# Performance work log

Measured on AMD Instinct MI355X. Metric: run time of the kernel, lower is better.

Reference implementation:

```python
import jax, jax.numpy as jnp
from jax import lax
import numpy as np

T, B, I, H = 365, 2048, 9, 50


def setup_inputs() -> dict:
    key = jax.random.key(0)
    ks = jax.random.split(key, 12)
    s = 0.1
    return {
        "x": jax.random.normal(ks[0], (T, B, I), dtype=jnp.float32),
        "w_ih0": jax.random.normal(ks[1], (4 * H, I), dtype=jnp.float32) * s,
        "w_hh0": jax.random.normal(ks[2], (4 * H, H), dtype=jnp.float32) * s,
        "b_ih0": jax.random.normal(ks[3], (4 * H,), dtype=jnp.float32) * s,
        "b_hh0": jax.random.normal(ks[4], (4 * H,), dtype=jnp.float32) * s,
        "w_ih1": jax.random.normal(ks[5], (4 * H, H), dtype=jnp.float32) * s,
        "w_hh1": jax.random.normal(ks[6], (4 * H, H), dtype=jnp.float32) * s,
        "b_ih1": jax.random.normal(ks[7], (4 * H,), dtype=jnp.float32) * s,
        "b_hh1": jax.random.normal(ks[8], (4 * H,), dtype=jnp.float32) * s,
        "fc_w": jax.random.normal(ks[9], (1, H), dtype=jnp.float32) * s,
        "fc_b": jax.random.normal(ks[10], (1,), dtype=jnp.float32) * s,
    }


def _lstm_layer(x, w_ih, w_hh, b_ih, b_hh):
    # x: [T, B, in]; PyTorch gate order: i, f, g, o
    Bq = x.shape[1]
    Hh = w_hh.shape[1]
    # precompute input projections for all timesteps (one big GEMM)
    x_proj = jnp.einsum('tbi,gi->tbg', x, w_ih) + b_ih + b_hh  # [T, B, 4H]

    def step(carry, xp):
        h, c = carry
        gates = xp + h @ w_hh.T  # [B, 4H]
        i, f, g, o = jnp.split(gates, 4, axis=-1)
        i = jax.nn.sigmoid(i)
        f = jax.nn.sigmoid(f)
        g = jnp.tanh(g)
        o = jax.nn.sigmoid(o)
        c = f * c + i * g
        h = o * jnp.tanh(c)
        return (h, c), h

    h0 = jnp.zeros((Bq, Hh), dtype=x.dtype)
    _, hs = lax.scan(step, (h0, h0), x_proj)
    return hs  # [T, B, H]


def reference(x, w_ih0, w_hh0, b_ih0, b_hh0, w_ih1, w_hh1, b_ih1, b_hh1, fc_w, fc_b):
    h1 = _lstm_layer(x, w_ih0, w_hh0, b_ih0, b_hh0)
    h2 = _lstm_layer(h1, w_ih1, w_hh1, b_ih1, b_hh1)
    out = jnp.einsum('tbh,oh->tbo', h2, fc_w) + fc_b  # [T, B, 1]
    return out
```

## Files before the change

### kernel.cpp

```cpp
#include <hip/hip_runtime.h>

#define T_STEPS 365
#define BATCH   2048
#define INP     9
#define HID     50
#define MB      16
#define NBLK    (BATCH/MB)
#define NT      512
#define NTILES  13

typedef __attribute__((ext_vector_type(8))) short short8;
typedef __attribute__((ext_vector_type(4))) float float4v;

__device__ __forceinline__ unsigned short f2bf(float v) {
    unsigned u = __builtin_bit_cast(unsigned, v);
    unsigned r = (u + 0x7FFFu + ((u >> 16) & 1u)) >> 16;
    return (unsigned short)r;
}
__device__ __forceinline__ float sig_(float x) {
    return __builtin_amdgcn_rcpf(1.f + __expf(-x));
}
__device__ __forceinline__ float tanh_(float x) {
    return 1.f - 2.f * __builtin_amdgcn_rcpf(__expf(2.f * x) + 1.f);
}

__device__ __forceinline__ int hx_off(int m, int k) {
    return (m * 128 + k) ^ ((m & 7) << 3);
}

__global__ __launch_bounds__(NT, 2)
void lstm_pipe(const float* __restrict__ x,
               const float* __restrict__ w_ih0, const float* __restrict__ w_hh0,
               const float* __restrict__ b_ih0, const float* __restrict__ b_hh0,
               const float* __restrict__ w_ih1, const float* __restrict__ w_hh1,
               const float* __restrict__ b_ih1, const float* __restrict__ b_hh1,
               const float* __restrict__ fc_w, const float* __restrict__ fc_b,
               float* __restrict__ out)
{
    __shared__ __align__(16) unsigned short HX[2][MB * 128];
    __shared__ float FCP[2][4][MB];

    const int t    = threadIdx.x;
    const int w    = t >> 6;
    const int lid  = t & 63;
    const int mcol = lid & 15;
    const int kgrp = lid >> 4;
    const int kb8  = kgrp * 8;
    const int b0   = blockIdx.x * MB;
    const bool isL1 = (w < 4);
    const int v    = isL1 ? w : (w - 4);
    const float fcb = fc_b[0];

    short8 wA[4][4];
    float  bs[4][4], fcw[4], cst[4];
    const float* bih = isL1 ? b_ih1 : b_ih0;
    const float* bhh = isL1 ? b_hh1 : b_hh0;

    #pragma unroll
    for (int tt = 0; tt < 4; ++tt) {
        const int T  = v + 4 * tt;
        const bool tv = (T < NTILES);
        const int r  = T * 16 + mcol;
        const bool rv = tv && (r < 4 * HID);
        const int u_r = r >> 2, g_r = r & 3;
        const int orig = g_r * HID + u_r;
        if (isL1) {
            #pragma unroll
            for (int kt = 0; kt < 4; ++kt) {
                short8 f;
                #pragma unroll
                for (int j = 0; j < 8; ++j) {
                    int k = kt * 32 + kb8 + j;
                    float val = 0.f;
                    if (rv) {
                        if (k < HID)                      val = w_ih1[orig * HID + k];
                        else if (k >= 64 && k < 64 + HID) val = w_hh1[orig * HID + (k - 64)];
                    }
                    f[j] = (short)f2bf(val);
                }
                wA[tt][kt] = f;
            }
        } else {
            #pragma unroll
            for (int kt = 0; kt < 2; ++kt) {
                short8 f;
                #pragma unroll
                for (int j = 0; j < 8; ++j) {
                    int k = kt * 32 + kb8 + j;
                    float val = 0.f;
                    if (rv) {
                        if (k < HID)            val = w_hh0[orig * HID + k];
                        else if (k < HID + INP) val = w_ih0[orig * INP + (k - HID)];
                    }
                    f[j] = (short)f2bf(val);
                }
                wA[tt][kt] = f;
            }
            wA[tt][2] = short8{}; wA[tt][3] = short8{};
        }
        const int u_lane = T * 4 + kgrp;
        #pragma unroll
        for (int rr = 0; rr < 4; ++rr) {
            int row = T * 16 + kgrp * 4 + rr;
            bool bvv = tv && (row < 4 * HID);
            int uu = row >> 2;
            bs[tt][rr] = bvv ? (bih[rr * HID + uu] + bhh[rr * HID + uu]) : 0.f;
        }
        fcw[tt] = (isL1 && tv && u_lane < HID) ? fc_w[u_lane] : 0.f;
        cst[tt] = 0.f;
    }

    int xi = -1;
    if (w == 4) xi = lid;
    else if (w == 5) xi = 64 + lid;
    else if (w == 6 && lid < 16) xi = 128 + lid;
    const bool xact = (xi >= 0 && xi < MB * INP);
    const int xm = xact ? xi / INP : 0, xj = xact ? xi % INP : 0;

    for (int i = t; i < 2 * MB * 128; i += NT) (&HX[0][0])[i] = 0;
    if (t < 2 * 4 * MB) (&FCP[0][0][0])[t] = 0.f;
    __syncthreads();
    float xreg = 0.f;
    if (xact) {
        HX[1][hx_off(xm, HID + xj)] = f2bf(x[(size_t)(b0 + xm) * INP + xj]);
        xreg = x[((size_t)BATCH + b0 + xm) * INP + xj];
    }
    __syncthreads();

    for (int ph = 0; ph < T_STEPS + 2; ++ph) {
        const int cur = (ph + 1) & 1, nxt = ph & 1;

        short8 f0 = *(const short8*)&HX[cur][hx_off(mcol, kb8)];
        short8 f1 = *(const short8*)&HX[cur][hx_off(mcol, 32 + kb8)];

        if (isL1) {
            if (ph >= 1 && ph <= T_STEPS) {
                short8 f2 = *(const short8*)&HX[cur][hx_off(mcol, 64 + kb8)];
                short8 f3 = *(const short8*)&HX[cur][hx_off(mcol, 96 + kb8)];
                float h1v[4];
                float fcp = 0.f;
                #pragma unroll
                for (int tt = 0; tt < 4; ++tt) {
                    const int T = v + 4 * tt;
                    if (T < NTILES) {
                        float4v acc = {bs[tt][0], bs[tt][1], bs[tt][2], bs[tt][3]};
                        acc = __builtin_amdgcn_mfma_f32_16x16x32_bf16(wA[tt][0], f0, acc, 0, 0, 0);
                        acc = __builtin_amdgcn_mfma_f32_16x16x32_bf16(wA[tt][1], f1, acc, 0, 0, 0);
                        acc = __builtin_amdgcn_mfma_f32_16x16x32_bf16(wA[tt][2], f2, acc, 0, 0, 0);
                        acc = __builtin_amdgcn_mfma_f32_16x16x32_bf16(wA[tt][3], f3, acc, 0, 0, 0);
                        float gi = sig_(acc[0]), gf = sig_(acc[1]);
                        float gg = tanh_(acc[2]), go = sig_(acc[3]);
                        cst[tt] = gf * cst[tt] + gi * gg;
                        h1v[tt] = go * tanh_(cst[tt]);
                        fcp += fcw[tt] * h1v[tt];
                    }
                }
                #pragma unroll
                for (int tt = 0; tt < 4; ++tt) {
                    const int T = v + 4 * tt, u = T * 4 + kgrp;
                    if (T < NTILES && u < HID)
                        HX[nxt][hx_off(mcol, 64 + u)] = f2bf(h1v[tt]);
                }
                fcp += __shfl_xor(fcp, 16);
                fcp += __shfl_xor(fcp, 32);
                if (lid < MB) FCP[ph & 1][v][lid] = fcp;
            }
        } else {
            if (ph < T_STEPS) {
                float h0v[4];
                #pragma unroll
                for (int tt = 0; tt < 4; ++tt) {
                    const int T = v + 4 * tt;
                    if (T < NTILES) {
                        float4v acc = {bs[tt][0], bs[tt][1], bs[tt][2], bs[tt][3]};
                        acc = __builtin_amdgcn_mfma_f32_16x16x32_bf16(wA[tt][0], f0, acc, 0, 0, 0);
                        acc = __builtin_amdgcn_mfma_f32_16x16x32_bf16(wA[tt][1], f1, acc, 0, 0, 0);
                        float gi = sig_(acc[0]), gf = sig_(acc[1]);
                        float gg = tanh_(acc[2]), go = sig_(acc[3]);
                        cst[tt] = gf * cst[tt] + gi * gg;
                        h0v[tt] = go * tanh_(cst[tt]);
                    }
                }
                #pragma unroll
                for (int tt = 0; tt < 4; ++tt) {
                    const int T = v + 4 * tt, u = T * 4 + kgrp;
                    if (T < NTILES && u < HID)
                        HX[nxt][hx_off(mcol, u)] = f2bf(h0v[tt]);
                }
            }
            if (xact) {
                if (ph + 1 < T_STEPS) HX[nxt][hx_off(xm, HID + xj)] = f2bf(xreg);
                if (ph + 2 < T_STEPS) xreg = x[((size_t)(ph + 2) * BATCH + b0 + xm) * INP + xj];
            }
            if (w == 7 && lid < MB && ph >= 2) {
                const int rp = (ph - 1) & 1;
                float s = fcb + FCP[rp][0][lid] + FCP[rp][1][lid]
                              + FCP[rp][2][lid] + FCP[rp][3][lid];
                out[(size_t)(ph - 2) * BATCH + b0 + lid] = s;
            }
        }
        __syncthreads();
    }
}

extern "C" void kernel_launch(void* const* d_in, const int* in_sizes, int n_in,
                              void* d_out, int out_size, void* d_ws, size_t ws_size,
                              hipStream_t stream) {
    const float* x     = (const float*)d_in[0];
    const float* w_ih0 = (const float*)d_in[1];
    const float* w_hh0 = (const float*)d_in[2];
    const float* b_ih0 = (const float*)d_in[3];
    const float* b_hh0 = (const float*)d_in[4];
    const float* w_ih1 = (const float*)d_in[5];
    const float* w_hh1 = (const float*)d_in[6];
    const float* b_ih1 = (const float*)d_in[7];
    const float* b_hh1 = (const float*)d_in[8];
    const float* fc_w  = (const float*)d_in[9];
    const float* fc_b  = (const float*)d_in[10];
    float* out = (float*)d_out;

    lstm_pipe<<<dim3(NBLK), dim3(NT), 0, stream>>>(
        x, w_ih0, w_hh0, b_ih0, b_hh0,
        w_ih1, w_hh1, b_ih1, b_hh1, fc_w, fc_b, out);
}
```

Baseline: 369.8 us.

## Double waves per block to shorten per-step serial tile chain

Blocks grow from 8 to 16 waves. Each layer now gets 8 waves, so each wave handles at most 2 gate tiles instead of 4, which shortens the serial MFMA and activation chain inside each timestep. The layer-1 MFMA chain is also split into two independent accumulators that are summed afterwards, to reduce dependency latency. In exchange the block is larger and the per-step barrier has more participants. The layer-0 waves also keep redundant zero weight registers, and the launch bound becomes (1024, 4), which tightens the per-thread register budget.

```diff
diff --git a/kernel.cpp b/kernel.cpp
--- a/kernel.cpp
+++ b/kernel.cpp
@@ -6,8 +6,9 @@
 #define HID     50
 #define MB      16
 #define NBLK    (BATCH/MB)
-#define NT      512
+#define NT      1024
 #define NTILES  13
+#define TPW     2
 
 typedef __attribute__((ext_vector_type(8))) short short8;
 typedef __attribute__((ext_vector_type(4))) float float4v;
@@ -28,17 +29,17 @@
     return (m * 128 + k) ^ ((m & 7) << 3);
 }
 
-__global__ __launch_bounds__(NT, 2)
-void lstm_pipe(const float* __restrict__ x,
-               const float* __restrict__ w_ih0, const float* __restrict__ w_hh0,
-               const float* __restrict__ b_ih0, const float* __restrict__ b_hh0,
-               const float* __restrict__ w_ih1, const float* __restrict__ w_hh1,
-               const float* __restrict__ b_ih1, const float* __restrict__ b_hh1,
-               const float* __restrict__ fc_w, const float* __restrict__ fc_b,
-               float* __restrict__ out)
+__global__ __launch_bounds__(NT, 4)
+void lstm_pipe16(const float* __restrict__ x,
+                 const float* __restrict__ w_ih0, const float* __restrict__ w_hh0,
+                 const float* __restrict__ b_ih0, const float* __restrict__ b_hh0,
+                 const float* __restrict__ w_ih1, const float* __restrict__ w_hh1,
+                 const float* __restrict__ b_ih1, const float* __restrict__ b_hh1,
+                 const float* __restrict__ fc_w, const float* __restrict__ fc_b,
+                 float* __restrict__ out)
 {
     __shared__ __align__(16) unsigned short HX[2][MB * 128];
-    __shared__ float FCP[2][4][MB];
+    __shared__ float FCP[2][8][MB];
 
     const int t    = threadIdx.x;
     const int w    = t >> 6;
@@ -47,56 +48,42 @@
     const int kgrp = lid >> 4;
     const int kb8  = kgrp * 8;
     const int b0   = blockIdx.x * MB;
-    const bool isL1 = (w < 4);
-    const int v    = isL1 ? w : (w - 4);
+    const bool isL1 = (w < 8);
+    const int v    = w & 7;
     const float fcb = fc_b[0];
 
-    short8 wA[4][4];
-    float  bs[4][4], fcw[4], cst[4];
+    short8 wA[TPW][4];
+    float  bs[TPW][4], fcw[TPW], cst[TPW];
     const float* bih = isL1 ? b_ih1 : b_ih0;
     const float* bhh = isL1 ? b_hh1 : b_hh0;
 
     #pragma unroll
-    for (int tt = 0; tt < 4; ++tt) {
-        const int T  = v + 4 * tt;
+    for (int tt = 0; tt < TPW; ++tt) {
+        const int T  = v + 8 * tt;
         const bool tv = (T < NTILES);
         const int r  = T * 16 + mcol;
         const bool rv = tv && (r < 4 * HID);
         const int u_r = r >> 2, g_r = r & 3;
         const int orig = g_r * HID + u_r;
-        if (isL1) {
+        #pragma unroll
+        for (int kt = 0; kt < 4; ++kt) {
+            short8 f;
             #pragma unroll
-            for (int kt = 0; kt < 4; ++kt) {
-                short8 f;
-                #pragma unroll
-                for (int j = 0; j < 8; ++j) {
-                    int k = kt * 32 + kb8 + j;
-                    float val = 0.f;
-                    if (rv) {
+            for (int j = 0; j < 8; ++j) {
+                int k = kt * 32 + kb8 + j;
+                float val = 0.f;
+                if (rv) {
+                    if (isL1) {
                         if (k < HID)                      val = w_ih1[orig * HID + k];
                         else if (k >= 64 && k < 64 + HID) val = w_hh1[orig * HID + (k - 64)];
-                    }
-                    f[j] = (short)f2bf(val);
-                }
-                wA[tt][kt] = f;
-            }
-        } else {
-            #pragma unroll
-            for (int kt = 0; kt < 2; ++kt) {
-                short8 f;
-                #pragma unroll
-                for (int j = 0; j < 8; ++j) {
-                    int k = kt * 32 + kb8 + j;
-                    float val = 0.f;
-                    if (rv) {
+                    } else {
                         if (k < HID)            val = w_hh0[orig * HID + k];
                         else if (k < HID + INP) val = w_ih0[orig * INP + (k - HID)];
                     }
-                    f[j] = (short)f2bf(val);
-                }
-                wA[tt][kt] = f;
-            }
-            wA[tt][2] = short8{}; wA[tt][3] = short8{};
+                }
+                f[j] = (short)f2bf(val);
+            }
+            wA[tt][kt] = f;
         }
         const int u_lane = T * 4 + kgrp;
         #pragma unroll
@@ -111,14 +98,14 @@
     }
 
     int xi = -1;
-    if (w == 4) xi = lid;
-    else if (w == 5) xi = 64 + lid;
-    else if (w == 6 && lid < 16) xi = 128 + lid;
+    if (w == 8) xi = lid;
+    else if (w == 9) xi = 64 + lid;
+    else if (w == 10 && lid < 16) xi = 128 + lid;
     const bool xact = (xi >= 0 && xi < MB * INP);
     const int xm = xact ? xi / INP : 0, xj = xact ? xi % INP : 0;
 
     for (int i = t; i < 2 * MB * 128; i += NT) (&HX[0][0])[i] = 0;
-    if (t < 2 * 4 * MB) (&FCP[0][0][0])[t] = 0.f;
+    if (t < 2 * 8 * MB) (&FCP[0][0][0])[t] = 0.f;
     __syncthreads();
     float xreg = 0.f;
     if (xact) {
@@ -137,27 +124,30 @@
             if (ph >= 1 && ph <= T_STEPS) {
                 short8 f2 = *(const short8*)&HX[cur][hx_off(mcol, 64 + kb8)];
                 short8 f3 = *(const short8*)&HX[cur][hx_off(mcol, 96 + kb8)];
-                float h1v[4];
+                float h1v[TPW];
                 float fcp = 0.f;
                 #pragma unroll
-                for (int tt = 0; tt < 4; ++tt) {
-                    const int T = v + 4 * tt;
+                for (int tt = 0; tt < TPW; ++tt) {
+                    const int T = v + 8 * tt;
                     if (T < NTILES) {
-                        float4v acc = {bs[tt][0], bs[tt][1], bs[tt][2], bs[tt][3]};
-                        acc = __builtin_amdgcn_mfma_f32_16x16x32_bf16(wA[tt][0], f0, acc, 0, 0, 0);
-                        acc = __builtin_amdgcn_mfma_f32_16x16x32_bf16(wA[tt][1], f1, acc, 0, 0, 0);
-                        acc = __builtin_amdgcn_mfma_f32_16x16x32_bf16(wA[tt][2], f2, acc, 0, 0, 0);
-                        acc = __builtin_amdgcn_mfma_f32_16x16x32_bf16(wA[tt][3], f3, acc, 0, 0, 0);
-                        float gi = sig_(acc[0]), gf = sig_(acc[1]);
-                        float gg = tanh_(acc[2]), go = sig_(acc[3]);
+                        float4v accA = {bs[tt][0], bs[tt][1], bs[tt][2], bs[tt][3]};
+                        float4v accB = {0.f, 0.f, 0.f, 0.f};
+                        accA = __builtin_amdgcn_mfma_f32_16x16x32_bf16(wA[tt][0], f0, accA, 0, 0, 0);
+                        accB = __builtin_amdgcn_mfma_f32_16x16x32_bf16(wA[tt][2], f2, accB, 0, 0, 0);
+                        accA = __builtin_amdgcn_mfma_f32_16x16x32_bf16(wA[tt][1], f1, accA, 0, 0, 0);
+                        accB = __builtin_amdgcn_mfma_f32_16x16x32_bf16(wA[tt][3], f3, accB, 0, 0, 0);
+                        float a0 = accA[0] + accB[0], a1 = accA[1] + accB[1];
+                        float a2 = accA[2] + accB[2], a3 = accA[3] + accB[3];
+                        float gi = sig_(a0), gf = sig_(a1);
+                        float gg = tanh_(a2), go = sig_(a3);
                         cst[tt] = gf * cst[tt] + gi * gg;
                         h1v[tt] = go * tanh_(cst[tt]);
                         fcp += fcw[tt] * h1v[tt];
                     }
                 }
                 #pragma unroll
-                for (int tt = 0; tt < 4; ++tt) {
-                    const int T = v + 4 * tt, u = T * 4 + kgrp;
+                for (int tt = 0; tt < TPW; ++tt) {
+                    const int T = v + 8 * tt, u = T * 4 + kgrp;
                     if (T < NTILES && u < HID)
                         HX[nxt][hx_off(mcol, 64 + u)] = f2bf(h1v[tt]);
                 }
@@ -167,10 +157,10 @@
             }
         } else {
             if (ph < T_STEPS) {
-                float h0v[4];
-                #pragma unroll
-                for (int tt = 0; tt < 4; ++tt) {
-                    const int T = v + 4 * tt;
+                float h0v[TPW];
+                #pragma unroll
+                for (int tt = 0; tt < TPW; ++tt) {
+                    const int T = v + 8 * tt;
                     if (T < NTILES) {
                         float4v acc = {bs[tt][0], bs[tt][1], bs[tt][2], bs[tt][3]};
                         acc = __builtin_amdgcn_mfma_f32_16x16x32_bf16(wA[tt][0], f0, acc, 0, 0, 0);
@@ -182,8 +172,8 @@
                     }
                 }
                 #pragma unroll
-                for (int tt = 0; tt < 4; ++tt) {
-                    const int T = v + 4 * tt, u = T * 4 + kgrp;
+                for (int tt = 0; tt < TPW; ++tt) {
+                    const int T = v + 8 * tt, u = T * 4 + kgrp;
                     if (T < NTILES && u < HID)
                         HX[nxt][hx_off(mcol, u)] = f2bf(h0v[tt]);
                 }
@@ -192,10 +182,11 @@
                 if (ph + 1 < T_STEPS) HX[nxt][hx_off(xm, HID + xj)] = f2bf(xreg);
                 if (ph + 2 < T_STEPS) xreg = x[((size_t)(ph + 2) * BATCH + b0 + xm) * INP + xj];
             }
-            if (w == 7 && lid < MB && ph >= 2) {
+            if (w == 15 && lid < MB && ph >= 2) {
                 const int rp = (ph - 1) & 1;
-                float s = fcb + FCP[rp][0][lid] + FCP[rp][1][lid]
-                              + FCP[rp][2][lid] + FCP[rp][3][lid];
+                float s = fcb;
+                #pragma unroll
+                for (int ww = 0; ww < 8; ++ww) s += FCP[rp][ww][lid];
                 out[(size_t)(ph - 2) * BATCH + b0 + lid] = s;
             }
         }
@@ -219,7 +210,7 @@
     const float* fc_b  = (const float*)d_in[10];
     float* out = (float*)d_out;
 
-    lstm_pipe<<<dim3(NBLK), dim3(NT), 0, stream>>>(
+    lstm_pipe16<<<dim3(NBLK), dim3(NT), 0, stream>>>(
         x, w_ih0, w_hh0, b_ih0, b_hh0,
         w_ih1, w_hh1, b_ih1, b_hh1, fc_w, fc_b, out);
 }
```

Result: faster. 354.2 us (-4.2%).

## Shrink per-block batch to four rows and split layer-1 MFMA accumulation chain

Applied to the files above, without the earlier changes.

Each block now handles 4 batch rows instead of 16, which quadruples the grid so it covers all CUs, and launch bounds are raised to allow more resident blocks. The MFMA tile stays 16 columns wide, so 12 of the 16 columns are zero padding and most of the matrix work is wasted. The layer-1 gate GEMM also splits its four chained MFMAs into two independent accumulators that are summed afterwards, to shorten the per-step dependency chain. The intent is to cut the latency-bound serial recurrence time by spreading batches across more CUs, at the cost of redundant compute and CU sharing between blocks.

```diff
diff --git a/kernel.cpp b/kernel.cpp
--- a/kernel.cpp
+++ b/kernel.cpp
@@ -4,10 +4,12 @@
 #define BATCH   2048
 #define INP     9
 #define HID     50
-#define MB      16
+#define MB      4
+#define MROW    16
 #define NBLK    (BATCH/MB)
 #define NT      512
 #define NTILES  13
+#define TPW     4
 
 typedef __attribute__((ext_vector_type(8))) short short8;
 typedef __attribute__((ext_vector_type(4))) float float4v;
@@ -28,16 +30,16 @@
     return (m * 128 + k) ^ ((m & 7) << 3);
 }
 
-__global__ __launch_bounds__(NT, 2)
-void lstm_pipe(const float* __restrict__ x,
-               const float* __restrict__ w_ih0, const float* __restrict__ w_hh0,
-               const float* __restrict__ b_ih0, const float* __restrict__ b_hh0,
-               const float* __restrict__ w_ih1, const float* __restrict__ w_hh1,
-               const float* __restrict__ b_ih1, const float* __restrict__ b_hh1,
-               const float* __restrict__ fc_w, const float* __restrict__ fc_b,
-               float* __restrict__ out)
+__global__ __launch_bounds__(NT, 4)
+void lstm_pipe2g(const float* __restrict__ x,
+                 const float* __restrict__ w_ih0, const float* __restrict__ w_hh0,
+                 const float* __restrict__ b_ih0, const float* __restrict__ b_hh0,
+                 const float* __restrict__ w_ih1, const float* __restrict__ w_hh1,
+                 const float* __restrict__ b_ih1, const float* __restrict__ b_hh1,
+                 const float* __restrict__ fc_w, const float* __restrict__ fc_b,
+                 float* __restrict__ out)
 {
-    __shared__ __align__(16) unsigned short HX[2][MB * 128];
+    __shared__ __align__(16) unsigned short HX[2][MROW * 128];
     __shared__ float FCP[2][4][MB];
 
     const int t    = threadIdx.x;
@@ -48,16 +50,16 @@
     const int kb8  = kgrp * 8;
     const int b0   = blockIdx.x * MB;
     const bool isL1 = (w < 4);
-    const int v    = isL1 ? w : (w - 4);
+    const int v    = w & 3;
     const float fcb = fc_b[0];
 
-    short8 wA[4][4];
-    float  bs[4][4], fcw[4], cst[4];
+    short8 wA[TPW][4];
+    float  bs[TPW][4], fcw[TPW], cst[TPW];
     const float* bih = isL1 ? b_ih1 : b_ih0;
     const float* bhh = isL1 ? b_hh1 : b_hh0;
 
     #pragma unroll
-    for (int tt = 0; tt < 4; ++tt) {
+    for (int tt = 0; tt < TPW; ++tt) {
         const int T  = v + 4 * tt;
         const bool tv = (T < NTILES);
         const int r  = T * 16 + mcol;
@@ -110,14 +112,10 @@
         cst[tt] = 0.f;
     }
 
-    int xi = -1;
-    if (w == 4) xi = lid;
-    else if (w == 5) xi = 64 + lid;
-    else if (w == 6 && lid < 16) xi = 128 + lid;
-    const bool xact = (xi >= 0 && xi < MB * INP);
-    const int xm = xact ? xi / INP : 0, xj = xact ? xi % INP : 0;
-
-    for (int i = t; i < 2 * MB * 128; i += NT) (&HX[0][0])[i] = 0;
+    const bool xact = (w == 4 && lid < MB * INP);
+    const int xm = xact ? lid / INP : 0, xj = xact ? lid % INP : 0;
+
+    for (int i = t; i < 2 * MROW * 128; i += NT) (&HX[0][0])[i] = 0;
     if (t < 2 * 4 * MB) (&FCP[0][0][0])[t] = 0.f;
     __syncthreads();
     float xreg = 0.f;
@@ -137,26 +135,29 @@
             if (ph >= 1 && ph <= T_STEPS) {
                 short8 f2 = *(const short8*)&HX[cur][hx_off(mcol, 64 + kb8)];
                 short8 f3 = *(const short8*)&HX[cur][hx_off(mcol, 96 + kb8)];
-                float h1v[4];
+                float h1v[TPW];
                 float fcp = 0.f;
                 #pragma unroll
-                for (int tt = 0; tt < 4; ++tt) {
+                for (int tt = 0; tt < TPW; ++tt) {
                     const int T = v + 4 * tt;
                     if (T < NTILES) {
-                        float4v acc = {bs[tt][0], bs[tt][1], bs[tt][2], bs[tt][3]};
-                        acc = __builtin_amdgcn_mfma_f32_16x16x32_bf16(wA[tt][0], f0, acc, 0, 0, 0);
-                        acc = __builtin_amdgcn_mfma_f32_16x16x32_bf16(wA[tt][1], f1, acc, 0, 0, 0);
-                        acc = __builtin_amdgcn_mfma_f32_16x16x32_bf16(wA[tt][2], f2, acc, 0, 0, 0);
-                        acc = __builtin_amdgcn_mfma_f32_16x16x32_bf16(wA[tt][3], f3, acc, 0, 0, 0);
-                        float gi = sig_(acc[0]), gf = sig_(acc[1]);
-                        float gg = tanh_(acc[2]), go = sig_(acc[3]);
+                        float4v accA = {bs[tt][0], bs[tt][1], bs[tt][2], bs[tt][3]};
+                        float4v accB = {0.f, 0.f, 0.f, 0.f};
+                        accA = __builtin_amdgcn_mfma_f32_16x16x32_bf16(wA[tt][0], f0, accA, 0, 0, 0);
+                        accB = __builtin_amdgcn_mfma_f32_16x16x32_bf16(wA[tt][2], f2, accB, 0, 0, 0);
+                        accA = __builtin_amdgcn_mfma_f32_16x16x32_bf16(wA[tt][1], f1, accA, 0, 0, 0);
+                        accB = __builtin_amdgcn_mfma_f32_16x16x32_bf16(wA[tt][3], f3, accB, 0, 0, 0);
+                        float a0 = accA[0] + accB[0], a1 = accA[1] + accB[1];
+                        float a2 = accA[2] + accB[2], a3 = accA[3] + accB[3];
+                        float gi = sig_(a0), gf = sig_(a1);
+                        float gg = tanh_(a2), go = sig_(a3);
                         cst[tt] = gf * cst[tt] + gi * gg;
                         h1v[tt] = go * tanh_(cst[tt]);
                         fcp += fcw[tt] * h1v[tt];
                     }
                 }
                 #pragma unroll
-                for (int tt = 0; tt < 4; ++tt) {
+                for (int tt = 0; tt < TPW; ++tt) {
                     const int T = v + 4 * tt, u = T * 4 + kgrp;
                     if (T < NTILES && u < HID)
                         HX[nxt][hx_off(mcol, 64 + u)] = f2bf(h1v[tt]);
@@ -167,9 +168,9 @@
             }
         } else {
             if (ph < T_STEPS) {
-                float h0v[4];
-                #pragma unroll
-                for (int tt = 0; tt < 4; ++tt) {
+                float h0v[TPW];
+                #pragma unroll
+                for (int tt = 0; tt < TPW; ++tt) {
                     const int T = v + 4 * tt;
                     if (T < NTILES) {
                         float4v acc = {bs[tt][0], bs[tt][1], bs[tt][2], bs[tt][3]};
@@ -182,7 +183,7 @@
                     }
                 }
                 #pragma unroll
-                for (int tt = 0; tt < 4; ++tt) {
+                for (int tt = 0; tt < TPW; ++tt) {
                     const int T = v + 4 * tt, u = T * 4 + kgrp;
                     if (T < NTILES && u < HID)
                         HX[nxt][hx_off(mcol, u)] = f2bf(h0v[tt]);
@@ -219,7 +220,7 @@
     const float* fc_b  = (const float*)d_in[10];
     float* out = (float*)d_out;
 
-    lstm_pipe<<<dim3(NBLK), dim3(NT), 0, stream>>>(
+    lstm_pipe2g<<<dim3(NBLK), dim3(NT), 0, stream>>>(
         x, w_ih0, w_hh0, b_ih0, b_hh0,
         w_ih1, w_hh1, b_ih1, b_hh1, fc_w, fc_b, out);
 }
```

Result: slower. 755.0 us (+104.2%).
